# Kernel tuning notes

Measured on AMD Instinct MI355X. Metric: run time of the kernel, lower is better.

The kernel has to match this reference:

```python
import jax, jax.numpy as jnp
import numpy as np

N = 8          # num merged RadialMLPs (experts)
D_IN = 64      # in_features
H = 128        # hidden_features
D_OUT = 64     # out_features
E = 100000     # num edges
LN_EPS = 1e-5


def setup_inputs() -> dict:
    key = jax.random.key(0)
    ks = jax.random.split(key, 12)
    s = lambda *shape: 0.05
    return {
        "x": jax.random.normal(ks[0], (E, D_IN), dtype=jnp.float32),
        # first layer concatenated across experts: [N*H, D_IN]
        "W1_cat": jax.random.normal(ks[1], (N * H, D_IN), dtype=jnp.float32) * 0.05,
        "b1_cat": jax.random.normal(ks[2], (N * H,), dtype=jnp.float32) * 0.05,
        "gamma1": jnp.ones((N, H), dtype=jnp.float32),
        "beta1": jnp.zeros((N, H), dtype=jnp.float32),
        "W2": jax.random.normal(ks[3], (N, H, H), dtype=jnp.float32) * 0.05,
        "b2": jax.random.normal(ks[4], (N, H), dtype=jnp.float32) * 0.05,
        "gamma2": jnp.ones((N, H), dtype=jnp.float32),
        "beta2": jnp.zeros((N, H), dtype=jnp.float32),
        "W3": jax.random.normal(ks[5], (N, D_OUT, H), dtype=jnp.float32) * 0.05,
        "b3": jax.random.normal(ks[6], (N, D_OUT), dtype=jnp.float32) * 0.05,
    }


def _layer_norm(h, gamma, beta):
    # h: [E, N, H]; gamma/beta: [N, H]; normalize over last dim (biased var)
    mu = jnp.mean(h, axis=-1, keepdims=True)
    var = jnp.mean(jnp.square(h - mu), axis=-1, keepdims=True)
    hn = (h - mu) * jax.lax.rsqrt(var + LN_EPS)
    return hn * gamma[None, :, :] + beta[None, :, :]


def reference(x, W1_cat, b1_cat, gamma1, beta1, W2, b2, gamma2, beta2, W3, b3):
    # Shared first GEMM: [E, D_IN] x [D_IN, N*H] -> [E, N, H]
    h = (x @ W1_cat.T + b1_cat).reshape(x.shape[0], N, H)
    h = jax.nn.silu(_layer_norm(h, gamma1, beta1))
    # Per-expert Linear 2, batched: W2 is [N, H_out, H_in]
    h = jnp.einsum("enh,nkh->enk", h, W2) + b2[None, :, :]
    h = jax.nn.silu(_layer_norm(h, gamma2, beta2))
    # Per-expert Linear 3: W3 is [N, D_OUT, H]
    out = jnp.einsum("enh,noh->eno", h, W3) + b3[None, :, :]
    # [N, E, D_OUT]: stack of the N per-expert outputs (original returns a list)
    return jnp.transpose(out, (1, 0, 2))
```

## Files before the change

kernel.cpp:

```cpp
#include <hip/hip_runtime.h>

#define NEXP 8
#define E_TOT 100000
#define EPB 64
#define NTILE 1563

typedef __bf16 bf16x8 __attribute__((ext_vector_type(8)));
typedef float f32x4 __attribute__((ext_vector_type(4)));
typedef unsigned short u16x8 __attribute__((ext_vector_type(8)));

union BF8 { u16x8 u; bf16x8 b; };
union BW  { __bf16 h; unsigned short u; };

__device__ __forceinline__ unsigned short f2bf(float f) {
  unsigned int u = __float_as_uint(f);
  u += 0x7fffu + ((u >> 16) & 1u);
  return (unsigned short)(u >> 16);
}

__device__ __forceinline__ int sidx(int r, int c, int stride) {
  return r * stride + (c ^ ((r & 7) << 3));
}

__device__ __forceinline__ bf16x8 fragld(const unsigned short* a, int off) {
  BF8 t;
  t.u = *(const u16x8*)(a + off);
  return t.b;
}

__device__ __forceinline__ bf16x8 frag_f32(const float* s) {
  float4 u0 = *(const float4*)s;
  float4 u1 = *(const float4*)(s + 4);
  BF8 t;
  t.u[0]=f2bf(u0.x); t.u[1]=f2bf(u0.y); t.u[2]=f2bf(u0.z); t.u[3]=f2bf(u0.w);
  t.u[4]=f2bf(u1.x); t.u[5]=f2bf(u1.y); t.u[6]=f2bf(u1.z); t.u[7]=f2bf(u1.w);
  return t.b;
}

__global__ void k_conv_w(const float* __restrict__ W1c, const float* __restrict__ W2p,
                         const float* __restrict__ W3p, unsigned short* __restrict__ wsW) {
  int gid = blockIdx.x * 256 + threadIdx.x;
  int n = gid >> 15, p = gid & 32767;
  int idx, frag, t, s, row;
  const float* base;
  int K;
  if (p < 8192)       { idx = p;         frag = idx >> 9; t = frag >> 1; s = frag & 1;
                        base = W1c + (size_t)n * 8192;  K = 64; }
  else if (p < 24576) { idx = p - 8192;  frag = idx >> 9; t = frag >> 2; s = frag & 3;
                        base = W2p + (size_t)n * 16384; K = 128; }
  else                { idx = p - 24576; frag = idx >> 9; t = frag >> 2; s = frag & 3;
                        base = W3p + (size_t)n * 8192;  K = 128; }
  int r = idx & 511, lane = r >> 3, j = r & 7;
  int l15 = lane & 15, gq = lane >> 4;
  row = (p < 24576) ? (16 * t + l15) : (4 * l15 + t);
  wsW[gid] = f2bf(base[row * K + 32 * s + 8 * gq + j]);
}

__global__ void k_conv_x(const float* __restrict__ xg, unsigned short* __restrict__ xb) {
  int gid = blockIdx.x * 256 + threadIdx.x;
  const float* s = xg + (size_t)gid * 8;
  BF8 t;
  float4 a = *(const float4*)s, b = *(const float4*)(s + 4);
  t.u[0]=f2bf(a.x); t.u[1]=f2bf(a.y); t.u[2]=f2bf(a.z); t.u[3]=f2bf(a.w);
  t.u[4]=f2bf(b.x); t.u[5]=f2bf(b.y); t.u[6]=f2bf(b.z); t.u[7]=f2bf(b.w);
  *(u16x8*)(xb + (size_t)gid * 8) = t.u;
}

template <bool USEWS>
__global__ __launch_bounds__(256, 3) void k_main(
    const unsigned short* __restrict__ wsW, const unsigned short* __restrict__ xb,
    const float* __restrict__ xg,
    const float* __restrict__ W1c, const float* __restrict__ b1c,
    const float* __restrict__ g1p, const float* __restrict__ bt1p,
    const float* __restrict__ W2p, const float* __restrict__ b2p,
    const float* __restrict__ g2p, const float* __restrict__ bt2p,
    const float* __restrict__ W3p, const float* __restrict__ b3p,
    float* __restrict__ outp)
{
  __shared__ __attribute__((aligned(16))) unsigned short hs[EPB * 128];

  const int bid = blockIdx.x;
  const int g_  = (bid & 7) * NTILE + (bid >> 3);
  const int tile = g_ >> 3;
  const int n    = g_ & 7;
  const int e0   = tile * EPB;

  const int tid  = threadIdx.x;
  const int lane = tid & 63;
  const int wv   = tid >> 6;
  const int l15  = lane & 15;
  const int gq   = lane >> 4;
  const int wrow = wv * 16;

  float b1v[8], g1v[8], bt1v[8], b2v[8], g2v[8], bt2v[8];
#pragma unroll
  for (int ct = 0; ct < 8; ++ct) {
    int col = n * 128 + ct * 16 + l15;
    b1v[ct] = b1c[col];  g1v[ct] = g1p[col];  bt1v[ct] = bt1p[col];
    b2v[ct] = b2p[col];  g2v[ct] = g2p[col];  bt2v[ct] = bt2p[col];
  }
  float4 b34 = *(const float4*)(b3p + n * 64 + 4 * l15);

  bf16x8 ax[2];
  {
    int e = e0 + wrow + l15;
    if (e >= E_TOT) e = E_TOT - 1;
    if (USEWS) {
#pragma unroll
      for (int s = 0; s < 2; ++s)
        ax[s] = fragld(xb, e * 64 + s * 32 + 8 * gq);
    } else {
#pragma unroll
      for (int s = 0; s < 2; ++s)
        ax[s] = frag_f32(xg + (size_t)e * 64 + s * 32 + 8 * gq);
    }
  }

  const unsigned short* wf1 = wsW + (size_t)n * 32768;
  const unsigned short* wf2 = wf1 + 8192;
  const unsigned short* wf3 = wf1 + 24576;
  const float* W1n = W1c + (size_t)n * 8192;
  const float* W2n = W2p + (size_t)n * 16384;
  const float* W3n = W3p + (size_t)n * 8192;

  auto wfrag = [&](const unsigned short* wf, const float* Wn, int fidx, int row, int s, int K) {
    if (USEWS) return fragld(wf, (fidx << 9) + (lane << 3));
    return frag_f32(Wn + row * K + 32 * s + 8 * gq);
  };

  f32x4 acc[8];

  auto ln_silu_store = [&](const float (&gv)[8], const float (&btv)[8]) {
    f32x4 sm4 = acc[0];
    f32x4 sq4 = acc[0] * acc[0];
#pragma unroll
    for (int ct = 1; ct < 8; ++ct) {
      f32x4 v = acc[ct];
      sm4 += v;
      sq4 += v * v;
    }
#pragma unroll
    for (int m = 1; m <= 8; m <<= 1) {
      f32x4 so, qo;
#pragma unroll
      for (int j = 0; j < 4; ++j) {
        so[j] = __shfl_xor(sm4[j], m);
        qo[j] = __shfl_xor(sq4[j], m);
      }
      sm4 += so;
      sq4 += qo;
    }
    f32x4 mu  = sm4 * (1.f / 128.f);
    f32x4 var = sq4 * (1.f / 128.f) - mu * mu;
    f32x4 rs;
#pragma unroll
    for (int j = 0; j < 4; ++j) rs[j] = __builtin_amdgcn_rsqf(var[j] + 1e-5f);
    int r0 = wrow + 4 * gq;
#pragma unroll
    for (int ct = 0; ct < 8; ++ct) {
      f32x4 t = (acc[ct] - mu) * rs;
#pragma unroll
      for (int j = 0; j < 4; ++j) {
        float v = t[j] * gv[ct] + btv[ct];
        v = v * __builtin_amdgcn_rcpf(1.f + __expf(-v));
        BW bw; bw.h = (__bf16)v;
        hs[sidx(r0 + j, ct * 16 + l15, 128)] = bw.u;
      }
    }
  };

#pragma unroll
  for (int ct = 0; ct < 8; ++ct) {
    float bv = b1v[ct];
    f32x4 b4 = {bv, bv, bv, bv};
    acc[ct] = b4;
  }
#pragma unroll
  for (int s = 0; s < 2; ++s) {
#pragma unroll
    for (int ct = 0; ct < 8; ++ct) {
      bf16x8 b = wfrag(wf1, W1n, ct * 2 + s, 16 * ct + l15, s, 64);
      acc[ct] = __builtin_amdgcn_mfma_f32_16x16x32_bf16(ax[s], b, acc[ct], 0, 0, 0);
    }
  }
  ln_silu_store(g1v, bt1v);

  f32x4 acc2[8];
#pragma unroll
  for (int ct = 0; ct < 8; ++ct) {
    float bv = b2v[ct];
    f32x4 b4 = {bv, bv, bv, bv};
    acc2[ct] = b4;
  }
#pragma unroll
  for (int ks = 0; ks < 4; ++ks) {
    bf16x8 a0 = fragld(hs, sidx(wrow + l15, ks * 32 + 8 * gq, 128));
#pragma unroll
    for (int ct = 0; ct < 8; ++ct) {
      bf16x8 b = wfrag(wf2, W2n, ct * 4 + ks, 16 * ct + l15, ks, 128);
      acc2[ct] = __builtin_amdgcn_mfma_f32_16x16x32_bf16(a0, b, acc2[ct], 0, 0, 0);
    }
  }
#pragma unroll
  for (int ct = 0; ct < 8; ++ct) acc[ct] = acc2[ct];
  ln_silu_store(g2v, bt2v);

  f32x4 a3[4];
#pragma unroll
  for (int t = 0; t < 4; ++t) {
    float bv = ((const float*)&b34)[t];
    f32x4 b4 = {bv, bv, bv, bv};
    a3[t] = b4;
  }
#pragma unroll
  for (int ks = 0; ks < 4; ++ks) {
    bf16x8 a0 = fragld(hs, sidx(wrow + l15, ks * 32 + 8 * gq, 128));
#pragma unroll
    for (int t = 0; t < 4; ++t) {
      bf16x8 b = wfrag(wf3, W3n, t * 4 + ks, 4 * l15 + t, ks, 128);
      a3[t] = __builtin_amdgcn_mfma_f32_16x16x32_bf16(a0, b, a3[t], 0, 0, 0);
    }
  }

#pragma unroll
  for (int j = 0; j < 4; ++j) {
    int e = e0 + wrow + 4 * gq + j;
    if (e < E_TOT) {
      float4 o4;
      o4.x = a3[0][j]; o4.y = a3[1][j]; o4.z = a3[2][j]; o4.w = a3[3][j];
      *(float4*)(outp + ((size_t)n * E_TOT + e) * 64 + 4 * l15) = o4;
    }
  }
}

extern "C" void kernel_launch(void* const* d_in, const int* in_sizes, int n_in,
                              void* d_out, int out_size, void* d_ws, size_t ws_size,
                              hipStream_t stream) {
  (void)in_sizes; (void)n_in; (void)out_size;
  const float* xg   = (const float*)d_in[0];
  const float* W1c  = (const float*)d_in[1];
  const float* b1c  = (const float*)d_in[2];
  const float* g1p  = (const float*)d_in[3];
  const float* bt1p = (const float*)d_in[4];
  const float* W2p  = (const float*)d_in[5];
  const float* b2p  = (const float*)d_in[6];
  const float* g2p  = (const float*)d_in[7];
  const float* bt2p = (const float*)d_in[8];
  const float* W3p  = (const float*)d_in[9];
  const float* b3p  = (const float*)d_in[10];
  float* outp = (float*)d_out;

  const size_t WS_W = (size_t)NEXP * 32768 * sizeof(unsigned short);
  const size_t WS_X = (size_t)E_TOT * 64 * sizeof(unsigned short);
  const bool usews = ws_size >= WS_W + WS_X;

  dim3 grid(NEXP * NTILE, 1, 1);
  dim3 block(256, 1, 1);

  if (usews) {
    unsigned short* wsW = (unsigned short*)d_ws;
    unsigned short* xb  = wsW + (size_t)NEXP * 32768;
    k_conv_w<<<1024, 256, 0, stream>>>(W1c, W2p, W3p, wsW);
    k_conv_x<<<3125, 256, 0, stream>>>(xg, xb);
    k_main<true><<<grid, block, 0, stream>>>(wsW, xb, xg, W1c, b1c, g1p, bt1p,
                                             W2p, b2p, g2p, bt2p, W3p, b3p, outp);
  } else {
    k_main<false><<<grid, block, 0, stream>>>(nullptr, nullptr, xg, W1c, b1c, g1p, bt1p,
                                              W2p, b2p, g2p, bt2p, W3p, b3p, outp);
  }
}
```

Measured before the change: 167.8 us.

## Process two 16-row tiles per wave to reuse weight fragments across rows

Doubles edges per block from 64 to 128, so each wave handles 32 rows as two 16-row MFMA tiles. Every weight fragment loaded for the three GEMMs is now used by two MFMAs instead of one, halving weight-load traffic per edge, and the block count is halved. The cost is twice the accumulator registers per thread (acc[2][8] plus a3[2][4]), which may lower occupancy, and a doubled LDS buffer for hs.

```diff
diff --git a/kernel.cpp b/kernel.cpp
--- a/kernel.cpp
+++ b/kernel.cpp
@@ -2,8 +2,8 @@
 
 #define NEXP 8
 #define E_TOT 100000
-#define EPB 64
-#define NTILE 1563
+#define EPB 128
+#define NTILE 782
 
 typedef __bf16 bf16x8 __attribute__((ext_vector_type(8)));
 typedef float f32x4 __attribute__((ext_vector_type(4)));
@@ -90,7 +90,7 @@
   const int wv   = tid >> 6;
   const int l15  = lane & 15;
   const int gq   = lane >> 4;
-  const int wrow = wv * 16;
+  const int wrow = wv * 32;
 
   float b1v[8], g1v[8], bt1v[8], b2v[8], g2v[8], bt2v[8];
 #pragma unroll
@@ -101,18 +101,19 @@
   }
   float4 b34 = *(const float4*)(b3p + n * 64 + 4 * l15);
 
-  bf16x8 ax[2];
-  {
-    int e = e0 + wrow + l15;
+  bf16x8 ax[2][2];
+#pragma unroll
+  for (int rt = 0; rt < 2; ++rt) {
+    int e = e0 + wrow + 16 * rt + l15;
     if (e >= E_TOT) e = E_TOT - 1;
     if (USEWS) {
 #pragma unroll
       for (int s = 0; s < 2; ++s)
-        ax[s] = fragld(xb, e * 64 + s * 32 + 8 * gq);
+        ax[rt][s] = fragld(xb, e * 64 + s * 32 + 8 * gq);
     } else {
 #pragma unroll
       for (int s = 0; s < 2; ++s)
-        ax[s] = frag_f32(xg + (size_t)e * 64 + s * 32 + 8 * gq);
+        ax[rt][s] = frag_f32(xg + (size_t)e * 64 + s * 32 + 8 * gq);
     }
   }
 
@@ -128,43 +129,46 @@
     return frag_f32(Wn + row * K + 32 * s + 8 * gq);
   };
 
-  f32x4 acc[8];
+  f32x4 acc[2][8];
 
   auto ln_silu_store = [&](const float (&gv)[8], const float (&btv)[8]) {
-    f32x4 sm4 = acc[0];
-    f32x4 sq4 = acc[0] * acc[0];
-#pragma unroll
-    for (int ct = 1; ct < 8; ++ct) {
-      f32x4 v = acc[ct];
-      sm4 += v;
-      sq4 += v * v;
-    }
-#pragma unroll
-    for (int m = 1; m <= 8; m <<= 1) {
-      f32x4 so, qo;
-#pragma unroll
-      for (int j = 0; j < 4; ++j) {
-        so[j] = __shfl_xor(sm4[j], m);
-        qo[j] = __shfl_xor(sq4[j], m);
-      }
-      sm4 += so;
-      sq4 += qo;
-    }
-    f32x4 mu  = sm4 * (1.f / 128.f);
-    f32x4 var = sq4 * (1.f / 128.f) - mu * mu;
-    f32x4 rs;
-#pragma unroll
-    for (int j = 0; j < 4; ++j) rs[j] = __builtin_amdgcn_rsqf(var[j] + 1e-5f);
-    int r0 = wrow + 4 * gq;
-#pragma unroll
-    for (int ct = 0; ct < 8; ++ct) {
-      f32x4 t = (acc[ct] - mu) * rs;
-#pragma unroll
-      for (int j = 0; j < 4; ++j) {
-        float v = t[j] * gv[ct] + btv[ct];
-        v = v * __builtin_amdgcn_rcpf(1.f + __expf(-v));
-        BW bw; bw.h = (__bf16)v;
-        hs[sidx(r0 + j, ct * 16 + l15, 128)] = bw.u;
+#pragma unroll
+    for (int rt = 0; rt < 2; ++rt) {
+      f32x4 sm4 = acc[rt][0];
+      f32x4 sq4 = acc[rt][0] * acc[rt][0];
+#pragma unroll
+      for (int ct = 1; ct < 8; ++ct) {
+        f32x4 v = acc[rt][ct];
+        sm4 += v;
+        sq4 += v * v;
+      }
+#pragma unroll
+      for (int m = 1; m <= 8; m <<= 1) {
+        f32x4 so, qo;
+#pragma unroll
+        for (int j = 0; j < 4; ++j) {
+          so[j] = __shfl_xor(sm4[j], m);
+          qo[j] = __shfl_xor(sq4[j], m);
+        }
+        sm4 += so;
+        sq4 += qo;
+      }
+      f32x4 mu  = sm4 * (1.f / 128.f);
+      f32x4 var = sq4 * (1.f / 128.f) - mu * mu;
+      f32x4 rs;
+#pragma unroll
+      for (int j = 0; j < 4; ++j) rs[j] = __builtin_amdgcn_rsqf(var[j] + 1e-5f);
+      int r0 = wrow + 16 * rt + 4 * gq;
+#pragma unroll
+      for (int ct = 0; ct < 8; ++ct) {
+        f32x4 t = (acc[rt][ct] - mu) * rs;
+#pragma unroll
+        for (int j = 0; j < 4; ++j) {
+          float v = t[j] * gv[ct] + btv[ct];
+          v = v * __builtin_amdgcn_rcpf(1.f + __expf(-v));
+          BW bw; bw.h = (__bf16)v;
+          hs[sidx(r0 + j, ct * 16 + l15, 128)] = bw.u;
+        }
       }
     }
   };
@@ -173,62 +177,71 @@
   for (int ct = 0; ct < 8; ++ct) {
     float bv = b1v[ct];
     f32x4 b4 = {bv, bv, bv, bv};
-    acc[ct] = b4;
+    acc[0][ct] = b4;
+    acc[1][ct] = b4;
   }
 #pragma unroll
   for (int s = 0; s < 2; ++s) {
 #pragma unroll
     for (int ct = 0; ct < 8; ++ct) {
       bf16x8 b = wfrag(wf1, W1n, ct * 2 + s, 16 * ct + l15, s, 64);
-      acc[ct] = __builtin_amdgcn_mfma_f32_16x16x32_bf16(ax[s], b, acc[ct], 0, 0, 0);
+      acc[0][ct] = __builtin_amdgcn_mfma_f32_16x16x32_bf16(ax[0][s], b, acc[0][ct], 0, 0, 0);
+      acc[1][ct] = __builtin_amdgcn_mfma_f32_16x16x32_bf16(ax[1][s], b, acc[1][ct], 0, 0, 0);
     }
   }
   ln_silu_store(g1v, bt1v);
 
-  f32x4 acc2[8];
 #pragma unroll
   for (int ct = 0; ct < 8; ++ct) {
     float bv = b2v[ct];
     f32x4 b4 = {bv, bv, bv, bv};
-    acc2[ct] = b4;
+    acc[0][ct] = b4;
+    acc[1][ct] = b4;
   }
 #pragma unroll
   for (int ks = 0; ks < 4; ++ks) {
-    bf16x8 a0 = fragld(hs, sidx(wrow + l15, ks * 32 + 8 * gq, 128));
+    bf16x8 a0 = fragld(hs, sidx(wrow + l15,      ks * 32 + 8 * gq, 128));
+    bf16x8 a1 = fragld(hs, sidx(wrow + 16 + l15, ks * 32 + 8 * gq, 128));
 #pragma unroll
     for (int ct = 0; ct < 8; ++ct) {
       bf16x8 b = wfrag(wf2, W2n, ct * 4 + ks, 16 * ct + l15, ks, 128);
-      acc2[ct] = __builtin_amdgcn_mfma_f32_16x16x32_bf16(a0, b, acc2[ct], 0, 0, 0);
-    }
-  }
-#pragma unroll
-  for (int ct = 0; ct < 8; ++ct) acc[ct] = acc2[ct];
+      acc[0][ct] = __builtin_amdgcn_mfma_f32_16x16x32_bf16(a0, b, acc[0][ct], 0, 0, 0);
+      acc[1][ct] = __builtin_amdgcn_mfma_f32_16x16x32_bf16(a1, b, acc[1][ct], 0, 0, 0);
+    }
+  }
   ln_silu_store(g2v, bt2v);
 
-  f32x4 a3[4];
+  f32x4 a3[2][4];
 #pragma unroll
   for (int t = 0; t < 4; ++t) {
     float bv = ((const float*)&b34)[t];
     f32x4 b4 = {bv, bv, bv, bv};
-    a3[t] = b4;
+    a3[0][t] = b4;
+    a3[1][t] = b4;
   }
 #pragma unroll
   for (int ks = 0; ks < 4; ++ks) {
-    bf16x8 a0 = fragld(hs, sidx(wrow + l15, ks * 32 + 8 * gq, 128));
+    bf16x8 a0 = fragld(hs, sidx(wrow + l15,      ks * 32 + 8 * gq, 128));
+    bf16x8 a1 = fragld(hs, sidx(wrow + 16 + l15, ks * 32 + 8 * gq, 128));
 #pragma unroll
     for (int t = 0; t < 4; ++t) {
       bf16x8 b = wfrag(wf3, W3n, t * 4 + ks, 4 * l15 + t, ks, 128);
-      a3[t] = __builtin_amdgcn_mfma_f32_16x16x32_bf16(a0, b, a3[t], 0, 0, 0);
-    }
-  }
-
-#pragma unroll
-  for (int j = 0; j < 4; ++j) {
-    int e = e0 + wrow + 4 * gq + j;
-    if (e < E_TOT) {
-      float4 o4;
-      o4.x = a3[0][j]; o4.y = a3[1][j]; o4.z = a3[2][j]; o4.w = a3[3][j];
-      *(float4*)(outp + ((size_t)n * E_TOT + e) * 64 + 4 * l15) = o4;
+      a3[0][t] = __builtin_amdgcn_mfma_f32_16x16x32_bf16(a0, b, a3[0][t], 0, 0, 0);
+      a3[1][t] = __builtin_amdgcn_mfma_f32_16x16x32_bf16(a1, b, a3[1][t], 0, 0, 0);
+    }
+  }
+
+#pragma unroll
+  for (int rt = 0; rt < 2; ++rt) {
+#pragma unroll
+    for (int j = 0; j < 4; ++j) {
+      int e = e0 + wrow + 16 * rt + 4 * gq + j;
+      if (e < E_TOT) {
+        float4 o4;
+        o4.x = a3[rt][0][j]; o4.y = a3[rt][1][j];
+        o4.z = a3[rt][2][j]; o4.w = a3[rt][3][j];
+        *(float4*)(outp + ((size_t)n * E_TOT + e) * 64 + 4 * l15) = o4;
+      }
     }
   }
 }
```

Measured after the change: 200.0 us. +19.2%, slower.
